# Performance work log

Hardware: AMD Instinct MI355X
Metric: run time of the kernel (lower is better)

The kernel has to match this reference:

```python
import jax, jax.numpy as jnp
import numpy as np
from functools import partial

NODES = 50
IN_SZ = 12
HID = 6


def _conv(x, W, b):
    # x: [N, C, H, W], W: [O, I, 3, 3], pad 1 -> same H, W
    y = jax.lax.conv_general_dilated(x, W, window_strides=(1, 1),
                                     padding=((1, 1), (1, 1)),
                                     dimension_numbers=('NCHW', 'OIHW', 'NCHW'))
    return y + b[None, :, None, None]


def setup_inputs() -> dict:
    key = jax.random.key(0)
    ks = jax.random.split(key, 12)
    B, T = 4096, 12
    d = {}
    d['A_hat'] = jax.random.normal(ks[0], (NODES, NODES), dtype=jnp.float32)
    d['X'] = jax.random.normal(ks[1], (B, NODES, T, IN_SZ, 1), dtype=jnp.float32)
    s_ih = 1.0 / np.sqrt(HID)
    d['W_ih'] = jax.random.uniform(ks[2], (4 * HID, IN_SZ), jnp.float32, -s_ih, s_ih)
    d['W_hh'] = jax.random.uniform(ks[3], (4 * HID, HID), jnp.float32, -s_ih, s_ih)
    d['b_ih'] = jax.random.uniform(ks[4], (4 * HID,), jnp.float32, -s_ih, s_ih)
    d['b_hh'] = jax.random.uniform(ks[5], (4 * HID,), jnp.float32, -s_ih, s_ih)
    d['Wf1'] = jax.random.normal(ks[6], (100, 50, 3, 3), jnp.float32) * 0.05
    d['bf1'] = jnp.zeros((100,), jnp.float32)
    d['Wf2'] = jax.random.normal(ks[7], (100, 100, 3, 3), jnp.float32) * 0.05
    d['bf2'] = jnp.zeros((100,), jnp.float32)
    d['Wf3'] = jax.random.normal(ks[8], (50, 100, 3, 3), jnp.float32) * 0.05
    d['bf3'] = jnp.zeros((50,), jnp.float32)
    d['W_lean'] = jax.random.normal(ks[9], (HID, HID), jnp.float32) * 0.3
    d['b_lean'] = jnp.zeros((HID,), jnp.float32)
    return d


def reference(A_hat, X, W_ih, W_hh, b_ih, b_hh, Wf1, bf1, Wf2, bf2, Wf3, bf3, W_lean, b_lean):
    # out1: [S, 50, 12] with S = B*T; the Python loop over S becomes a scan
    out1 = jnp.squeeze(X, axis=4).reshape(-1, NODES, IN_SZ)

    def step(carry, x_t):
        h, c = carry  # each [50, 6]
        gates = x_t @ W_ih.T + b_ih + h @ W_hh.T + b_hh  # [50, 24]
        i, f, g, o = jnp.split(gates, 4, axis=-1)
        i = jax.nn.sigmoid(i)
        f = jax.nn.sigmoid(f)
        g = jnp.tanh(g)
        o = jax.nn.sigmoid(o)
        c_new = f * c + i * g
        h_new = o * jnp.tanh(c_new)
        h_new = jnp.tanh(h_new)  # module applies extra tanh and feeds it back
        return (h_new, c_new), h_new

    h0 = jnp.zeros((NODES, HID), dtype=X.dtype)
    c0 = jnp.zeros((NODES, HID), dtype=X.dtype)
    _, al = jax.lax.scan(step, (h0, c0), out1)  # al: [S, 50, 6]

    out2 = al.reshape(-1, NODES, HID, 1)  # [S, 50, 6, 1]
    f = jax.nn.relu(_conv(out2, Wf1, bf1))
    f = jax.nn.relu(_conv(f, Wf2, bf2))
    f = jax.nn.relu(_conv(f, Wf3, bf3))
    out = (f.reshape(-1, HID) @ W_lean.T + b_lean).reshape(-1, NODES, HID, 1)
    return out
```

## Files before the change

kernel.cpp:

```cpp
#include <hip/hip_runtime.h>

#define NCH 1024
#define CL 48
#define WM 16

typedef _Float16 half8 __attribute__((ext_vector_type(8)));
typedef float f32x4 __attribute__((ext_vector_type(4)));

#define ROWB 256
#define BUFB 17408
#define ALH_OFF 131072

__device__ __forceinline__ int swz(int srow, int b){ return srow*ROWB + (b ^ ((srow&7)<<4)); }

__device__ __forceinline__ unsigned short f2h_bits(float x){
  _Float16 h = (_Float16)x;
  return __builtin_bit_cast(unsigned short, h);
}

__device__ __forceinline__ float rcp_(float x){ return __builtin_amdgcn_rcpf(x); }
__device__ __forceinline__ float tanh_(float z){ return 1.f - 2.f*rcp_(1.f + __expf(2.f*z)); }

__global__ void pack_frags(const float* __restrict__ W1, const float* __restrict__ W2,
                           const float* __restrict__ W3, unsigned short* __restrict__ ws)
{
  int tid = blockIdx.x*256 + threadIdx.x;
  if (tid >= 174*512) return;
  int f = tid >> 9, e = tid & 511, l = e >> 3, j = e & 7;
  int d, ks, nt, I, O; const float* W;
  if (f < 42)      { int x = f;     int st = x/7;  nt = x%7; d = st/2; ks = st%2; I = 50;  O = 100; W = W1; }
  else if (f < 126){ int x = f-42;  int st = x/7;  nt = x%7; d = st/4; ks = st%4; I = 100; O = 100; W = W2; }
  else             { int x = f-126; int st = x/4;  nt = x%4; d = st/4; ks = st%4; I = 100; O = 50;  W = W3; }
  int k = ks*32 + ((l>>4)<<3) + j;
  int o = nt*16 + (l&15);
  float v = (k < I && o < O) ? W[((o*I + k)*3 + d)*3 + 1] : 0.f;
  ws[tid] = f2h_bits(v);
}

template<bool F16>
__global__ __launch_bounds__(128,3) void lstm_scan2(
    const float* __restrict__ X, const float* __restrict__ Wih,
    const float* __restrict__ Whh, const float* __restrict__ bih,
    const float* __restrict__ bhh, float* __restrict__ al32,
    unsigned short* __restrict__ al16)
{
  const int l = threadIdx.x & 63;
  const int wv = threadIdx.x >> 6;
  const int blk = blockIdx.x;
  const int p4 = blk/5, w = blk - p4*5;
  const int q = l/6, j = l - q*6;
  const bool active = (q < 10);
  const int n = w*10 + (active ? q : 0);
  const int sbase = active ? q*6 : 0;

  const int c0 = p4*4 + 2*wv;
  const int sAb = c0*CL, sBb = sAb + CL;
  const int sALast = sAb + CL - 1, sBLast = sBb + CL - 1;

  float wi[4][12], wh[4][6], bb[4];
  #pragma unroll
  for (int g=0; g<4; ++g){
    const int r = g*6 + j;
    const float4 w0 = *(const float4*)(Wih + r*12);
    const float4 w1 = *(const float4*)(Wih + r*12 + 4);
    const float4 w2 = *(const float4*)(Wih + r*12 + 8);
    wi[g][0]=w0.x; wi[g][1]=w0.y; wi[g][2]=w0.z; wi[g][3]=w0.w;
    wi[g][4]=w1.x; wi[g][5]=w1.y; wi[g][6]=w1.z; wi[g][7]=w1.w;
    wi[g][8]=w2.x; wi[g][9]=w2.y; wi[g][10]=w2.z; wi[g][11]=w2.w;
    const float2 h0 = *(const float2*)(Whh + r*6);
    const float2 h1 = *(const float2*)(Whh + r*6 + 2);
    const float2 h2 = *(const float2*)(Whh + r*6 + 4);
    wh[g][0]=h0.x; wh[g][1]=h0.y; wh[g][2]=h1.x;
    wh[g][3]=h1.y; wh[g][4]=h2.x; wh[g][5]=h2.y;
    bb[g] = bih[r] + bhh[r];
  }

  float hA[6], hB[6], cA = 0.f, cB = 0.f;
  #pragma unroll
  for (int k=0;k<6;++k){ hA[k]=0.f; hB[k]=0.f; }

  const int sA0 = (c0==0) ? 0 : (sAb - WM);
  const int sB0 = sBb - WM;
  float4 xA0,xA1,xA2, xB0,xB1,xB2;
  { const float4* pa = (const float4*)(X + (size_t)sA0*600 + n*12); xA0=pa[0]; xA1=pa[1]; xA2=pa[2]; }
  { const float4* pb = (const float4*)(X + (size_t)sB0*600 + n*12); xB0=pb[0]; xB1=pb[1]; xB2=pb[2]; }

  auto step = [&](const float4& x0, const float4& x1, const float4& x2,
                  float* h, float& c) -> float {
    const float xr[12] = {x0.x,x0.y,x0.z,x0.w, x1.x,x1.y,x1.z,x1.w, x2.x,x2.y,x2.z,x2.w};
    float a0=bb[0], a1=bb[1], a2=bb[2], a3=bb[3];
    #pragma unroll
    for (int k=0;k<12;++k){ a0+=wi[0][k]*xr[k]; a1+=wi[1][k]*xr[k];
                            a2+=wi[2][k]*xr[k]; a3+=wi[3][k]*xr[k]; }
    #pragma unroll
    for (int k=0;k<6;++k){ a0+=wh[0][k]*h[k]; a1+=wh[1][k]*h[k];
                           a2+=wh[2][k]*h[k]; a3+=wh[3][k]*h[k]; }
    const float gi = rcp_(1.f + __expf(-a0));
    const float gf = rcp_(1.f + __expf(-a1));
    const float gg = 2.f*rcp_(1.f + __expf(-(a2+a2))) - 1.f;
    const float go = rcp_(1.f + __expf(-a3));
    c = gf*c + gi*gg;
    return tanh_(go * tanh_(c));
  };

  for (int i = -WM; i < CL; ++i){
    const int sA = sAb + i, sB = sBb + i;
    const bool doA = (sA >= 0);
    float4 yA0,yA1,yA2, yB0,yB1,yB2;
    { const int sn = (sB < sBLast) ? sB+1 : sBLast;
      const float4* xq = (const float4*)(X + (size_t)sn*600 + n*12);
      yB0=xq[0]; yB1=xq[1]; yB2=xq[2]; }
    if (doA){
      const int sn = (sA < sALast) ? sA+1 : sALast;
      const float4* xq = (const float4*)(X + (size_t)sn*600 + n*12);
      yA0=xq[0]; yA1=xq[1]; yA2=xq[2];
    }

    float hnA = 0.f;
    if (doA) hnA = step(xA0,xA1,xA2, hA, cA);
    const float hnB = step(xB0,xB1,xB2, hB, cB);

    if (active && i >= 0){
      const size_t oA = (size_t)sA*300 + n*6 + j;
      const size_t oB = (size_t)sB*300 + n*6 + j;
      if (F16){ al16[oA] = f2h_bits(hnA); al16[oB] = f2h_bits(hnB); }
      else    { al32[oA] = hnA;           al32[oB] = hnB; }
    }
    #pragma unroll
    for (int k=0;k<6;++k){
      hA[k] = __shfl(hnA, sbase + k, 64);
      hB[k] = __shfl(hnB, sbase + k, 64);
    }
    if (doA){ xA0=yA0; xA1=yA1; xA2=yA2; }
    xB0=yB0; xB1=yB1; xB2=yB2;
  }
}

template<int KS, int NTT, int NTG, bool LAST>
__device__ __forceinline__ void conv_layer2(
    char* lds, int inOff, int outOff, const unsigned short* __restrict__ wsU,
    int fbase, int ntOff, const float* __restrict__ bias, int O, int m0, int lane)
{
  f32x4 acc[2][NTG];
  #pragma unroll
  for (int m=0;m<2;m++)
    #pragma unroll
    for (int n=0;n<NTG;n++) acc[m][n] = (f32x4){0.f,0.f,0.f,0.f};

  const int ar = m0 + (lane & 15);
  const int abyte_g = (lane>>4)<<4;
  const int laneb = lane << 3;

  half8 a0c = *(const half8*)(lds + inOff + swz(ar, abyte_g));
  half8 a1c = *(const half8*)(lds + inOff + swz(ar + 16, abyte_g));
  half8 bc[NTG];
  {
    const unsigned short* p0 = wsU + (size_t)(fbase + ntOff)*512 + laneb;
    #pragma unroll
    for (int n=0;n<NTG;n++) bc[n] = *(const half8*)(p0 + n*512);
  }

  #pragma unroll
  for (int st=0; st<3*KS; ++st){
    half8 a0n, a1n, bn[NTG];
    if (st+1 < 3*KS){
      const int dn = (st+1)/KS, ksn = (st+1)%KS;
      a0n = *(const half8*)(lds + inOff + swz(ar + dn, ksn*64 + abyte_g));
      a1n = *(const half8*)(lds + inOff + swz(ar + 16 + dn, ksn*64 + abyte_g));
      const unsigned short* pn = wsU + (size_t)(fbase + (st+1)*NTT + ntOff)*512 + laneb;
      #pragma unroll
      for (int n=0;n<NTG;n++) bn[n] = *(const half8*)(pn + n*512);
    }
    #pragma unroll
    for (int n=0;n<NTG;n++){
      acc[0][n] = __builtin_amdgcn_mfma_f32_16x16x32_f16(a0c, bc[n], acc[0][n], 0, 0, 0);
      acc[1][n] = __builtin_amdgcn_mfma_f32_16x16x32_f16(a1c, bc[n], acc[1][n], 0, 0, 0);
    }
    if (st+1 < 3*KS){
      a0c = a0n; a1c = a1n;
      #pragma unroll
      for (int n=0;n<NTG;n++) bc[n] = bn[n];
    }
  }

  const int colBase = lane & 15;
  #pragma unroll
  for (int m=0;m<2;m++){
    const int rbase = m0 + m*16 + ((lane>>4)<<2);
    #pragma unroll
    for (int n=0;n<NTG;n++){
      const int col = (ntOff + n)*16 + colBase;
      if (col < O){
        const float b = bias[col];
        #pragma unroll
        for (int r=0;r<4;r++){
          const int crow = rbase + r;
          const int p8 = crow & 7;
          if (p8 >= 1 && p8 <= 6){
            const float v = fmaxf(acc[m][n][r] + b, 0.f);
            const int srow = crow + 1;
            if (LAST) *(float*)(lds + outOff + swz(srow, col*4)) = v;
            else      *(unsigned short*)(lds + outOff + swz(srow, col*2)) = f2h_bits(v);
          }
        }
      }
    }
  }
}

template<int KS, int NTT, int NTG>
__device__ __forceinline__ void conv_layer3_fused(
    char* lds, int inOff, const unsigned short* __restrict__ wsU,
    int fbase, int ntOff, const float* __restrict__ b3,
    const float* __restrict__ Wl, const float* __restrict__ bl,
    float* __restrict__ io, size_t base, int m0, int lane)
{
  f32x4 acc[2][NTG];
  #pragma unroll
  for (int m=0;m<2;m++)
    #pragma unroll
    for (int n=0;n<NTG;n++) acc[m][n] = (f32x4){0.f,0.f,0.f,0.f};

  const int ar = m0 + (lane & 15);
  const int abyte_g = (lane>>4)<<4;
  const int laneb = lane << 3;

  half8 a0c = *(const half8*)(lds + inOff + swz(ar, abyte_g));
  half8 a1c = *(const half8*)(lds + inOff + swz(ar + 16, abyte_g));
  half8 bc[NTG];
  {
    const unsigned short* p0 = wsU + (size_t)(fbase + ntOff)*512 + laneb;
    #pragma unroll
    for (int n=0;n<NTG;n++) bc[n] = *(const half8*)(p0 + n*512);
  }

  #pragma unroll
  for (int st=0; st<3*KS; ++st){
    half8 a0n, a1n, bn[NTG];
    if (st+1 < 3*KS){
      const int dn = (st+1)/KS, ksn = (st+1)%KS;
      a0n = *(const half8*)(lds + inOff + swz(ar + dn, ksn*64 + abyte_g));
      a1n = *(const half8*)(lds + inOff + swz(ar + 16 + dn, ksn*64 + abyte_g));
      const unsigned short* pn = wsU + (size_t)(fbase + (st+1)*NTT + ntOff)*512 + laneb;
      #pragma unroll
      for (int n=0;n<NTG;n++) bn[n] = *(const half8*)(pn + n*512);
    }
    #pragma unroll
    for (int n=0;n<NTG;n++){
      acc[0][n] = __builtin_amdgcn_mfma_f32_16x16x32_f16(a0c, bc[n], acc[0][n], 0, 0, 0);
      acc[1][n] = __builtin_amdgcn_mfma_f32_16x16x32_f16(a1c, bc[n], acc[1][n], 0, 0, 0);
    }
    if (st+1 < 3*KS){
      a0c = a0n; a1c = a1n;
      #pragma unroll
      for (int n=0;n<NTG;n++) bc[n] = bn[n];
    }
  }

  const int colBase = lane & 15;
  const int qg = lane >> 4;
  const bool hiHalf = (qg & 1);
  #pragma unroll
  for (int m=0;m<2;m++){
    const int sIdx = (m0 + m*16 + qg*4) >> 3;
    #pragma unroll
    for (int n=0;n<NTG;n++){
      const int col = (ntOff + n)*16 + colBase;
      const bool valid = (col < 50);
      const float b = valid ? b3[col] : 0.f;
      float vv[4];
      #pragma unroll
      for (int r=0;r<4;r++) vv[r] = fmaxf(acc[m][n][r] + b, 0.f);
      float tot[6];
      #pragma unroll
      for (int j=0;j<6;j++){
        float pj;
        if (!hiHalf) pj = Wl[j*6+0]*vv[1] + Wl[j*6+1]*vv[2] + Wl[j*6+2]*vv[3];
        else         pj = Wl[j*6+3]*vv[0] + Wl[j*6+4]*vv[1] + Wl[j*6+5]*vv[2];
        tot[j] = pj + __shfl_xor(pj, 16, 64);
      }
      if (valid && !hiHalf){
        float* dst = io + base + (size_t)sIdx*300 + col*6;
        float2 p0 = {tot[0]+bl[0], tot[1]+bl[1]};
        float2 p1 = {tot[2]+bl[2], tot[3]+bl[3]};
        float2 p2 = {tot[4]+bl[4], tot[5]+bl[5]};
        *(float2*)(dst+0) = p0;
        *(float2*)(dst+2) = p1;
        *(float2*)(dst+4) = p2;
      }
    }
  }
}

template<bool ALH>
__global__ __launch_bounds__(256,4) void conv_mfma_kernel(
    float* __restrict__ io, const unsigned short* __restrict__ alh,
    const unsigned short* __restrict__ wsU,
    const float* __restrict__ b1, const float* __restrict__ b2, const float* __restrict__ b3,
    const float* __restrict__ Wl, const float* __restrict__ bl)
{
  __shared__ __align__(16) char lds[2*BUFB];
  const int t = threadIdx.x;
  const int lane = t & 63, w = t >> 6;
  const int mg = w >> 1, ng = w & 1;
  const int m0 = mg*32;
  const size_t base = (size_t)blockIdx.x * 2400;

  for (int i = t; i < (2*BUFB)/16; i += 256) ((f32x4*)lds)[i] = (f32x4){0.f,0.f,0.f,0.f};
  __syncthreads();

  if (ALH){
    const unsigned short* ap = alh + base;
    for (int idx = t; idx < 400; idx += 256){
      const int s = idx/50, n = idx - (idx/50)*50;
      const unsigned short* pp = ap + s*300 + n*6;
      const int r0 = s*8 + 2;
      #pragma unroll
      for (int y=0; y<6; ++y)
        *(unsigned short*)(lds + swz(r0 + y, n*2)) = pp[y];
    }
  } else {
    for (int idx = t; idx < 2400; idx += 256){
      const float v = io[base + idx];
      const int s = idx/300, rr = idx%300;
      const int ch = rr/6, y = rr%6;
      *(unsigned short*)(lds + swz(s*8 + y + 2, ch*2)) = f2h_bits(v);
    }
  }
  __syncthreads();

  if (ng == 0) conv_layer2<2,7,4,false>(lds, 0,    BUFB, wsU, 0,   0, b1, 100, m0, lane);
  else         conv_layer2<2,7,3,false>(lds, 0,    BUFB, wsU, 0,   4, b1, 100, m0, lane);
  __syncthreads();
  if (ng == 0) conv_layer2<4,7,4,false>(lds, BUFB, 0,    wsU, 42,  0, b2, 100, m0, lane);
  else         conv_layer2<4,7,3,false>(lds, BUFB, 0,    wsU, 42,  4, b2, 100, m0, lane);
  __syncthreads();
  if (ng == 0) conv_layer3_fused<4,4,2>(lds, 0, wsU, 126, 0, b3, Wl, bl, io, base, m0, lane);
  else         conv_layer3_fused<4,4,2>(lds, 0, wsU, 126, 2, b3, Wl, bl, io, base, m0, lane);
}

__device__ __forceinline__ float wraw(const float* __restrict__ W, int I, int i, int d, int o){
  return W[((o*I + i)*3 + d)*3 + 1];
}
template<int NS>
__device__ void conv_layer_valu(const float (* __restrict__ in)[100][8],
                                float (* __restrict__ outb)[100][8],
                                int I, const float* __restrict__ W,
                                const float* __restrict__ bias, int o, int s0)
{
  float acc[NS][6];
  const float b = bias[o];
  #pragma unroll
  for (int s=0;s<NS;s++)
    #pragma unroll
    for (int y=0;y<6;y++) acc[s][y]=b;
  for (int i=0;i<I;i++){
    const float w0 = wraw(W,I,i,0,o), w1 = wraw(W,I,i,1,o), w2 = wraw(W,I,i,2,o);
    #pragma unroll
    for (int s=0;s<NS;s++){
      const float4 r0 = *(const float4*)&in[s0+s][i][0];
      const float4 r1 = *(const float4*)&in[s0+s][i][4];
      acc[s][0] += w1*r0.x + w2*r0.y;
      acc[s][1] += w0*r0.x + w1*r0.y + w2*r0.z;
      acc[s][2] += w0*r0.y + w1*r0.z + w2*r0.w;
      acc[s][3] += w0*r0.z + w1*r0.w + w2*r1.x;
      acc[s][4] += w0*r0.w + w1*r1.x + w2*r1.y;
      acc[s][5] += w0*r1.x + w1*r1.y;
    }
  }
  #pragma unroll
  for (int s=0;s<NS;s++){
    float4 v0; float2 v1;
    v0.x = fmaxf(acc[s][0],0.f); v0.y = fmaxf(acc[s][1],0.f);
    v0.z = fmaxf(acc[s][2],0.f); v0.w = fmaxf(acc[s][3],0.f);
    v1.x = fmaxf(acc[s][4],0.f); v1.y = fmaxf(acc[s][5],0.f);
    *(float4*)&outb[s0+s][o][0] = v0;
    *(float2*)&outb[s0+s][o][4] = v1;
  }
}
__global__ __launch_bounds__(256,1) void conv_kernel_fb(
    float* __restrict__ io,
    const float* __restrict__ W1, const float* __restrict__ b1,
    const float* __restrict__ W2, const float* __restrict__ b2,
    const float* __restrict__ W3, const float* __restrict__ b3,
    const float* __restrict__ Wl, const float* __restrict__ bl)
{
  __shared__ float A[8][100][8];
  __shared__ float B[8][100][8];
  const int t = threadIdx.x;
  const size_t base = (size_t)blockIdx.x * 2400;
  for (int idx=t; idx<800; idx+=256){
    const int s = idx/100, ch = idx%100;
    A[s][ch][6]=0.f; A[s][ch][7]=0.f; B[s][ch][6]=0.f; B[s][ch][7]=0.f;
  }
  for (int idx=t; idx<2400; idx+=256){
    const float v = io[base + idx];
    const int s = idx/300, rr = idx%300;
    A[s][rr/6][rr%6] = v;
  }
  __syncthreads();
  const int w = t>>6, lane = t&63;
  { const int sh = w>>1, o = (w&1)*50 + lane;
    if (lane < 50) conv_layer_valu<4>(A, B, 50, W1, b1, o, sh*4); }
  __syncthreads();
  { const int sh = w>>1, o = (w&1)*50 + lane;
    if (lane < 50) conv_layer_valu<4>(B, A, 100, W2, b2, o, sh*4); }
  __syncthreads();
  { if (lane < 50) conv_layer_valu<2>(A, B, 100, W3, b3, lane, w*2); }
  __syncthreads();
  for (int idx=t; idx<2400; idx+=256){
    const int s = idx/300, rr = idx%300, n = rr/6, j = rr%6;
    const float4 r0 = *(const float4*)&B[s][n][0];
    const float2 r1 = *(const float2*)&B[s][n][4];
    io[base + idx] = bl[j] + Wl[j*6+0]*r0.x + Wl[j*6+1]*r0.y + Wl[j*6+2]*r0.z
                   + Wl[j*6+3]*r0.w + Wl[j*6+4]*r1.x + Wl[j*6+5]*r1.y;
  }
}

extern "C" void kernel_launch(void* const* d_in, const int* in_sizes, int n_in,
                              void* d_out, int out_size, void* d_ws, size_t ws_size,
                              hipStream_t stream)
{
  const float* X    = (const float*)d_in[1];
  const float* Wih  = (const float*)d_in[2];
  const float* Whh  = (const float*)d_in[3];
  const float* bih  = (const float*)d_in[4];
  const float* bhh  = (const float*)d_in[5];
  const float* Wf1  = (const float*)d_in[6];
  const float* bf1  = (const float*)d_in[7];
  const float* Wf2  = (const float*)d_in[8];
  const float* bf2  = (const float*)d_in[9];
  const float* Wf3  = (const float*)d_in[10];
  const float* bf3  = (const float*)d_in[11];
  const float* Wl   = (const float*)d_in[12];
  const float* bl   = (const float*)d_in[13];
  float* out = (float*)d_out;
  unsigned short* wsU = (unsigned short*)d_ws;

  const bool packed = (ws_size >= 174*512*sizeof(unsigned short));
  const bool bigws  = (ws_size >= (size_t)(ALH_OFF + 49152ull*300ull)*2ull);

  if (packed)
    hipLaunchKernelGGL(pack_frags, dim3(348), dim3(256), 0, stream,
                       Wf1, Wf2, Wf3, wsU);

  if (bigws && packed){
    unsigned short* alh = wsU + ALH_OFF;
    hipLaunchKernelGGL((lstm_scan2<true>), dim3((NCH/4)*5), dim3(128), 0, stream,
                       X, Wih, Whh, bih, bhh, nullptr, alh);
    hipLaunchKernelGGL((conv_mfma_kernel<true>), dim3(6144), dim3(256), 0, stream,
                       out, alh, wsU, bf1, bf2, bf3, Wl, bl);
  } else {
    hipLaunchKernelGGL((lstm_scan2<false>), dim3((NCH/4)*5), dim3(128), 0, stream,
                       X, Wih, Whh, bih, bhh, out, nullptr);
    if (packed)
      hipLaunchKernelGGL((conv_mfma_kernel<false>), dim3(6144), dim3(256), 0, stream,
                         out, nullptr, wsU, bf1, bf2, bf3, Wl, bl);
    else
      hipLaunchKernelGGL(conv_kernel_fb, dim3(6144), dim3(256), 0, stream,
                         out, Wf1, bf1, Wf2, bf2, Wf3, bf3, Wl, bl);
  }
}
```

Baseline: 209.6 us.

## Store fp16 LSTM outputs transposed to enable vectorized conv LDS staging

The fp16 LSTM output buffer is now written in hidden-major order (j*50+n) for each step instead of node-major. The conv kernel can then copy each 100-byte row of 50 channels with 16-byte loads straight into its swizzled LDS rows, replacing scattered 2-byte loads and stores. The cost is that the LSTM's fp16 stores become strided per lane, and both kernels now depend on the new layout agreement.

```diff
diff --git a/kernel.cpp b/kernel.cpp
--- a/kernel.cpp
+++ b/kernel.cpp
@@ -6,6 +6,7 @@
 
 typedef _Float16 half8 __attribute__((ext_vector_type(8)));
 typedef float f32x4 __attribute__((ext_vector_type(4)));
+typedef unsigned uint4a __attribute__((ext_vector_type(4), aligned(4)));
 
 #define ROWB 256
 #define BUFB 17408
@@ -52,6 +53,7 @@
   const bool active = (q < 10);
   const int n = w*10 + (active ? q : 0);
   const int sbase = active ? q*6 : 0;
+  const int off16 = j*50 + n;
 
   const int c0 = p4*4 + 2*wv;
   const int sAb = c0*CL, sBb = sAb + CL;
@@ -121,10 +123,13 @@
     const float hnB = step(xB0,xB1,xB2, hB, cB);
 
     if (active && i >= 0){
-      const size_t oA = (size_t)sA*300 + n*6 + j;
-      const size_t oB = (size_t)sB*300 + n*6 + j;
-      if (F16){ al16[oA] = f2h_bits(hnA); al16[oB] = f2h_bits(hnB); }
-      else    { al32[oA] = hnA;           al32[oB] = hnB; }
+      if (F16){
+        al16[(size_t)sA*300 + off16] = f2h_bits(hnA);
+        al16[(size_t)sB*300 + off16] = f2h_bits(hnB);
+      } else {
+        al32[(size_t)sA*300 + n*6 + j] = hnA;
+        al32[(size_t)sB*300 + n*6 + j] = hnB;
+      }
     }
     #pragma unroll
     for (int k=0;k<6;++k){
@@ -310,14 +315,19 @@
   __syncthreads();
 
   if (ALH){
-    const unsigned short* ap = alh + base;
-    for (int idx = t; idx < 400; idx += 256){
-      const int s = idx/50, n = idx - (idx/50)*50;
-      const unsigned short* pp = ap + s*300 + n*6;
-      const int r0 = s*8 + 2;
-      #pragma unroll
-      for (int y=0; y<6; ++y)
-        *(unsigned short*)(lds + swz(r0 + y, n*2)) = pp[y];
+    const char* ap = (const char*)(alh + base);
+    for (int idx = t; idx < 336; idx += 256){
+      const int ri = idx/7, c = idx - ri*7;
+      const int s = ri/6, j = ri - s*6;
+      const int row = s*8 + 2 + j;
+      const char* src = ap + s*600 + j*100;
+      if (c < 6){
+        uint4a v = *(const uint4a*)(src + c*16);
+        *(uint4a*)(lds + swz(row, c*16)) = v;
+      } else {
+        unsigned v = *(const unsigned*)(src + 96);
+        *(unsigned*)(lds + swz(row, 96)) = v;
+      }
     }
   } else {
     for (int idx = t; idx < 2400; idx += 256){
```

Result: no change. 209.1 us (-0.3%).
